# Kernel optimization log

Hardware: AMD Instinct MI355X
Metric: run time of the kernel (lower is better)

The kernel has to match this reference:

```python
import jax, jax.numpy as jnp
import numpy as np
from jax import lax

N_EXPERTS = 16
TOP_K = 2
D_MODEL = 512
D_FF = 2048


def setup_inputs() -> dict:
    key = jax.random.key(0)
    ks = jax.random.split(key, 7)
    s_in = 1.0 / np.sqrt(D_MODEL)
    s_ff = 1.0 / np.sqrt(D_FF)
    x = jax.random.normal(ks[0], (2, 2048, D_MODEL), dtype=jnp.float32)
    router_w = jax.random.uniform(ks[1], (N_EXPERTS, D_MODEL), jnp.float32, -s_in, s_in)
    router_b = jax.random.uniform(ks[2], (N_EXPERTS,), jnp.float32, -s_in, s_in)
    w1 = jax.random.uniform(ks[3], (N_EXPERTS, D_FF, D_MODEL), jnp.float32, -s_in, s_in)
    b1 = jax.random.uniform(ks[4], (N_EXPERTS, D_FF), jnp.float32, -s_in, s_in)
    w2 = jax.random.uniform(ks[5], (N_EXPERTS, D_MODEL, D_FF), jnp.float32, -s_ff, s_ff)
    b2 = jax.random.uniform(ks[6], (N_EXPERTS, D_MODEL), jnp.float32, -s_ff, s_ff)
    return {"x": x, "router_w": router_w, "router_b": router_b,
            "w1": w1, "b1": b1, "w2": w2, "b2": b2}


def reference(x, router_w, router_b, w1, b1, w2, b2):
    B, S, D = x.shape
    xt = x.reshape(-1, D)                                   # [T, D]
    logits = xt @ router_w.T + router_b                     # [T, E]
    probs = jax.nn.softmax(logits, axis=-1)
    topk_p, topk_i = lax.top_k(probs, TOP_K)                # [T, K]
    # Dense gate matrix: gate[t, e] = topk prob if expert e selected else 0.
    # Weighting by gate reproduces the masked gather/scatter-add exactly.
    onehot = jax.nn.one_hot(topk_i, N_EXPERTS, dtype=probs.dtype)  # [T, K, E]
    gates = jnp.sum(onehot * topk_p[..., None], axis=1)     # [T, E]

    def expert_step(acc, packed):
        w1e, b1e, w2e, b2e, ge = packed                     # per-expert params + gate col [T]
        h = jax.nn.gelu(xt @ w1e.T + b1e, approximate=False)  # [T, D_FF]
        y = h @ w2e.T + b2e                                 # [T, D]
        return acc + y * ge[:, None], None

    out, _ = lax.scan(expert_step, jnp.zeros_like(xt),
                      (w1, b1, w2, b2, gates.T))
    return out.reshape(B, S, D)
```

## Files before the change

kernel.cpp:

```cpp
#include <hip/hip_runtime.h>
#include <stdint.h>

#define T_TOK 4096
#define DM    512
#define DFF   2048
#define NE    16
#define NSLOT (T_TOK * 2)
#define NW    (NE * DFF * DM)
#define MAXTILE 80

typedef __attribute__((ext_vector_type(8))) short  bf16x8;
typedef __attribute__((ext_vector_type(4))) float  f32x4;
typedef __attribute__((ext_vector_type(8))) unsigned short us8;

static __device__ __forceinline__ unsigned short f2bf(float f) {
    unsigned int u = __float_as_uint(f);
    u += 0x7FFFu + ((u >> 16) & 1u);
    return (unsigned short)(u >> 16);
}

static __device__ __forceinline__ void gload_lds16(const void* g, void* l) {
    __builtin_amdgcn_global_load_lds(
        (const __attribute__((address_space(1))) void*)g,
        (__attribute__((address_space(3))) void*)l, 16, 0, 0);
}

__global__ __launch_bounds__(256) void convert_kernel(
    const float* __restrict__ w1, const float* __restrict__ w2,
    unsigned short* __restrict__ w1b, unsigned short* __restrict__ w2b)
{
    size_t i = ((size_t)blockIdx.x * 256 + threadIdx.x) * 8;
    const float* src; unsigned short* dst;
    if (i < (size_t)NW) { src = w1 + i;        dst = w1b + i; }
    else                { src = w2 + (i - NW); dst = w2b + (i - NW); }
    f32x4 a = *(const f32x4*)src;
    f32x4 b = *(const f32x4*)(src + 4);
    us8 v;
    v[0] = f2bf(a.x); v[1] = f2bf(a.y); v[2] = f2bf(a.z); v[3] = f2bf(a.w);
    v[4] = f2bf(b.x); v[5] = f2bf(b.y); v[6] = f2bf(b.z); v[7] = f2bf(b.w);
    *(us8*)dst = v;
}

__global__ __launch_bounds__(256) void router_kernel(
    const float* __restrict__ x, const float* __restrict__ rw,
    const float* __restrict__ rb, int* __restrict__ tok_e,
    float* __restrict__ tok_g, unsigned short* __restrict__ xb)
{
    __shared__ float rws[NE * DM];
    int tid = threadIdx.x;
    for (int i = 0; i < 8; ++i) {
        int idx = (tid + i * 256) * 4;
        *(f32x4*)&rws[idx] = *(const f32x4*)&rw[idx];
    }
    __syncthreads();

    int wid = tid >> 6, lane = tid & 63;
    int t = blockIdx.x * 4 + wid;

    float xv[8];
    const float* xp = x + (size_t)t * DM + lane * 8;
    *(f32x4*)&xv[0] = *(const f32x4*)xp;
    *(f32x4*)&xv[4] = *(const f32x4*)(xp + 4);

    us8 v;
    for (int i = 0; i < 8; ++i) v[i] = f2bf(xv[i]);
    *(us8*)&xb[(size_t)t * DM + lane * 8] = v;

    float acc[NE];
    for (int e = 0; e < NE; ++e) {
        const float* wp = &rws[e * DM + lane * 8];
        float a = 0.f;
        for (int i = 0; i < 8; ++i) a += xv[i] * wp[i];
        acc[e] = a;
    }
    for (int e = 0; e < NE; ++e) {
        float v2 = acc[e];
        for (int off = 32; off > 0; off >>= 1) v2 += __shfl_xor(v2, off);
        acc[e] = v2 + rb[e];
    }
    float m = acc[0];
    for (int e = 1; e < NE; ++e) m = fmaxf(m, acc[e]);
    float p[NE]; float s = 0.f;
    for (int e = 0; e < NE; ++e) { p[e] = expf(acc[e] - m); s += p[e]; }
    float inv = 1.f / s;
    int i0 = 0; float p0 = p[0];
    for (int e = 1; e < NE; ++e) if (p[e] > p0) { p0 = p[e]; i0 = e; }
    int i1 = (i0 == 0) ? 1 : 0; float p1 = p[i1];
    for (int e = 0; e < NE; ++e)
        if (e != i0 && p[e] > p1) { p1 = p[e]; i1 = e; }
    if (lane == 0) {
        tok_e[t * 2]     = i0;  tok_e[t * 2 + 1] = i1;
        tok_g[t * 2]     = p0 * inv;
        tok_g[t * 2 + 1] = p1 * inv;
    }
}

__global__ __launch_bounds__(256) void compact_kernel(
    const int* __restrict__ tok_e, int* __restrict__ slot_token,
    int* __restrict__ tok_slot, int* __restrict__ eoff)
{
    __shared__ int cnt[NE], cur[NE];
    int tid = threadIdx.x;
    if (tid < NE) cnt[tid] = 0;
    __syncthreads();
    for (int t = tid; t < T_TOK; t += 256) {
        atomicAdd(&cnt[tok_e[t * 2]], 1);
        atomicAdd(&cnt[tok_e[t * 2 + 1]], 1);
    }
    __syncthreads();
    if (tid == 0) {
        int r = 0, tb = 0;
        for (int e = 0; e < NE; ++e) {
            eoff[e] = r; cur[e] = r; r += cnt[e];
            eoff[16 + e] = cnt[e];
            eoff[32 + e] = tb; tb += (cnt[e] + 127) >> 7;
        }
        eoff[48] = tb;
    }
    __syncthreads();
    for (int t = tid; t < T_TOK; t += 256) {
        for (int k = 0; k < 2; ++k) {
            int e = tok_e[t * 2 + k];
            int s = atomicAdd(&cur[e], 1);
            slot_token[s]     = t;
            tok_slot[t * 2 + k] = s;
        }
    }
}

__global__ __launch_bounds__(256) void gemm1_kernel(
    const unsigned short* __restrict__ xb, const unsigned short* __restrict__ w1b,
    const float* __restrict__ b1, const int* __restrict__ slot_token,
    const int* __restrict__ eoff, unsigned short* __restrict__ h)
{
    __shared__ unsigned short smem[16384];
    __shared__ int tokrow[128];
    __shared__ int meta[49];
    unsigned short* As = smem;
    unsigned short* Bs = smem + 8192;

    int tid = threadIdx.x;
    if (tid < 49) meta[tid] = eoff[tid];
    __syncthreads();

    int slot_idx = blockIdx.y;
    if (slot_idx >= meta[48]) return;
    int e = 0;
    while (e < NE - 1 && meta[32 + e + 1] <= slot_idx) ++e;
    int mt  = slot_idx - meta[32 + e];
    int off = meta[e], cnt = meta[16 + e];
    int nB    = blockIdx.x * 128;
    int slot0 = off + mt * 128;
    int valid = cnt - mt * 128; if (valid > 128) valid = 128;

    if (tid < 128) {
        int s = slot0 + tid; if (s > NSLOT - 1) s = NSLOT - 1;
        tokrow[tid] = slot_token[s];
    }
    __syncthreads();

    f32x4 acc[16];
    for (int i = 0; i < 16; ++i) acc[i] = (f32x4){0.f, 0.f, 0.f, 0.f};

    const unsigned short* wb = w1b + ((size_t)e * DFF + nB) * DM;
    int wid = tid >> 6, l = tid & 63;
    int wm = (wid & 1) * 64, wn = (wid >> 1) * 64;
    int q = l >> 4, c = l & 15;

    for (int kt = 0; kt < DM / 64; ++kt) {
        for (int j = 0; j < 4; ++j) {
            int u = (wid * 4 + j) * 64 + l;
            int row = u >> 3, sc = (u & 7) ^ (row & 7);
            gload_lds16(xb + (size_t)tokrow[row] * DM + kt * 64 + sc * 8, &As[u * 8]);
        }
        for (int j = 0; j < 4; ++j) {
            int u = (wid * 4 + j) * 64 + l;
            int row = u >> 3, sc = (u & 7) ^ (row & 7);
            gload_lds16(wb + (size_t)row * DM + kt * 64 + sc * 8, &Bs[u * 8]);
        }
        __syncthreads();
        for (int ks = 0; ks < 2; ++ks) {
            int sw = ((ks * 4 + q) ^ (c & 7)) * 8;
            bf16x8 af[4], bv[4];
            for (int i = 0; i < 4; ++i) af[i] = *(bf16x8*)&As[(wm + i * 16 + c) * 64 + sw];
            for (int j = 0; j < 4; ++j) bv[j] = *(bf16x8*)&Bs[(wn + j * 16 + c) * 64 + sw];
            for (int i = 0; i < 4; ++i)
                for (int j = 0; j < 4; ++j)
                    acc[i * 4 + j] = __builtin_amdgcn_mfma_f32_16x16x32_bf16(
                        af[i], bv[j], acc[i * 4 + j], 0, 0, 0);
        }
        __syncthreads();
    }

    float bias[4];
    for (int j = 0; j < 4; ++j) bias[j] = b1[e * DFF + nB + wn + j * 16 + c];
    unsigned short* bounce = smem;
    for (int ph = 0; ph < 2; ++ph) {
        __syncthreads();
        if ((wid & 1) == ph) {
            for (int i = 0; i < 4; ++i)
                for (int j = 0; j < 4; ++j) {
                    f32x4 a = acc[i * 4 + j];
                    for (int r = 0; r < 4; ++r) {
                        int rl = i * 16 + q * 4 + r;
                        float z = a[r] + bias[j];
                        float g = 0.5f * z * (1.f + erff(z * 0.70710678118654752f));
                        bounce[rl * 136 + wn + j * 16 + c] = f2bf(g);
                    }
                }
        }
        __syncthreads();
        for (int it = 0; it < 4; ++it) {
            int u2 = it * 256 + tid;
            int row = u2 >> 4, ch = u2 & 15;
            int gr = ph * 64 + row;
            if (gr < valid)
                *(us8*)&h[(size_t)(slot0 + gr) * DFF + nB + ch * 8] =
                    *(us8*)&bounce[row * 136 + ch * 8];
        }
    }
}

__global__ __launch_bounds__(256) void gemm2_kernel(
    const unsigned short* __restrict__ h, const unsigned short* __restrict__ w2b,
    const int* __restrict__ eoff, float* __restrict__ y)
{
    __shared__ unsigned short smem[16384];
    __shared__ int meta[49];
    unsigned short* As = smem;
    unsigned short* Bs = smem + 8192;

    int tid = threadIdx.x;
    if (tid < 49) meta[tid] = eoff[tid];
    __syncthreads();

    int slot_idx = blockIdx.y;
    if (slot_idx >= meta[48]) return;
    int e = 0;
    while (e < NE - 1 && meta[32 + e + 1] <= slot_idx) ++e;
    int mt  = slot_idx - meta[32 + e];
    int off = meta[e], cnt = meta[16 + e];
    int nB    = blockIdx.x * 128;
    int slot0 = off + mt * 128;
    int valid = cnt - mt * 128; if (valid > 128) valid = 128;

    f32x4 acc[16];
    for (int i = 0; i < 16; ++i) acc[i] = (f32x4){0.f, 0.f, 0.f, 0.f};

    const unsigned short* wb = w2b + ((size_t)e * DM + nB) * DFF;
    int wid = tid >> 6, l = tid & 63;
    int wm = (wid & 1) * 64, wn = (wid >> 1) * 64;
    int q = l >> 4, c = l & 15;

    for (int kt = 0; kt < DFF / 64; ++kt) {
        for (int j = 0; j < 4; ++j) {
            int u = (wid * 4 + j) * 64 + l;
            int row = u >> 3, sc = (u & 7) ^ (row & 7);
            size_t s = slot0 + row; if (s > NSLOT - 1) s = NSLOT - 1;
            gload_lds16(h + s * DFF + kt * 64 + sc * 8, &As[u * 8]);
        }
        for (int j = 0; j < 4; ++j) {
            int u = (wid * 4 + j) * 64 + l;
            int row = u >> 3, sc = (u & 7) ^ (row & 7);
            gload_lds16(wb + (size_t)row * DFF + kt * 64 + sc * 8, &Bs[u * 8]);
        }
        __syncthreads();
        for (int ks = 0; ks < 2; ++ks) {
            int sw = ((ks * 4 + q) ^ (c & 7)) * 8;
            bf16x8 af[4], bv[4];
            for (int i = 0; i < 4; ++i) af[i] = *(bf16x8*)&As[(wm + i * 16 + c) * 64 + sw];
            for (int j = 0; j < 4; ++j) bv[j] = *(bf16x8*)&Bs[(wn + j * 16 + c) * 64 + sw];
            for (int i = 0; i < 4; ++i)
                for (int j = 0; j < 4; ++j)
                    acc[i * 4 + j] = __builtin_amdgcn_mfma_f32_16x16x32_bf16(
                        af[i], bv[j], acc[i * 4 + j], 0, 0, 0);
        }
        __syncthreads();
    }

    for (int i = 0; i < 4; ++i)
        for (int j = 0; j < 4; ++j) {
            int n = nB + wn + j * 16 + c;
            for (int r = 0; r < 4; ++r) {
                int rl = wm + i * 16 + q * 4 + r;
                if (rl < valid)
                    y[(size_t)(slot0 + rl) * DM + n] = acc[i * 4 + j][r];
            }
        }
}

__global__ __launch_bounds__(256) void combine_kernel(
    const float* __restrict__ y, const float* __restrict__ b2,
    const int* __restrict__ tok_slot, const float* __restrict__ tok_g,
    const int* __restrict__ tok_e, float* __restrict__ out)
{
    int tid = threadIdx.x;
    int t = blockIdx.x * 2 + (tid >> 7);
    int d = (tid & 127) * 4;
    int s0 = tok_slot[t * 2], s1 = tok_slot[t * 2 + 1];
    float g0 = tok_g[t * 2], g1 = tok_g[t * 2 + 1];
    int e0 = tok_e[t * 2], e1 = tok_e[t * 2 + 1];
    f32x4 y0 = *(const f32x4*)&y[(size_t)s0 * DM + d];
    f32x4 y1 = *(const f32x4*)&y[(size_t)s1 * DM + d];
    f32x4 c0 = *(const f32x4*)&b2[e0 * DM + d];
    f32x4 c1 = *(const f32x4*)&b2[e1 * DM + d];
    f32x4 o;
    for (int i = 0; i < 4; ++i) o[i] = g0 * (y0[i] + c0[i]) + g1 * (y1[i] + c1[i]);
    *(f32x4*)&out[(size_t)t * DM + d] = o;
}

extern "C" void kernel_launch(void* const* d_in, const int* in_sizes, int n_in,
                              void* d_out, int out_size, void* d_ws, size_t ws_size,
                              hipStream_t stream) {
    const float* x  = (const float*)d_in[0];
    const float* rw = (const float*)d_in[1];
    const float* rb = (const float*)d_in[2];
    const float* w1 = (const float*)d_in[3];
    const float* b1 = (const float*)d_in[4];
    const float* w2 = (const float*)d_in[5];
    const float* b2 = (const float*)d_in[6];
    float* out = (float*)d_out;

    char* ws = (char*)d_ws;
    size_t o = 0;
    unsigned short* h   = (unsigned short*)(ws + o); o += (size_t)NSLOT * DFF * 2;
    unsigned short* w1b = (unsigned short*)(ws + o); o += (size_t)NW * 2;
    unsigned short* w2b = (unsigned short*)(ws + o); o += (size_t)NW * 2;
    unsigned short* xb  = (unsigned short*)(ws + o); o += (size_t)T_TOK * DM * 2;
    int*   tok_e      = (int*)(ws + o);   o += (size_t)NSLOT * 4;
    float* tok_g      = (float*)(ws + o); o += (size_t)NSLOT * 4;
    int*   tok_slot   = (int*)(ws + o);   o += (size_t)NSLOT * 4;
    int*   slot_token = (int*)(ws + o);   o += (size_t)NSLOT * 4;
    int*   eoff       = (int*)(ws + o);
    float* y = (float*)w1b;

    convert_kernel<<<2 * NW / 8 / 256, 256, 0, stream>>>(w1, w2, w1b, w2b);
    router_kernel<<<T_TOK / 4, 256, 0, stream>>>(x, rw, rb, tok_e, tok_g, xb);
    compact_kernel<<<1, 256, 0, stream>>>(tok_e, slot_token, tok_slot, eoff);
    gemm1_kernel<<<dim3(DFF / 128, MAXTILE), 256, 0, stream>>>(
        xb, w1b, b1, slot_token, eoff, h);
    gemm2_kernel<<<dim3(DM / 128, MAXTILE), 256, 0, stream>>>(
        h, w2b, eoff, y);
    combine_kernel<<<T_TOK / 2, 256, 0, stream>>>(
        y, b2, tok_slot, tok_g, tok_e, out);
}
```

Measured before the change: 315.8 us.

## Replace LDS-staged expert GEMMs with direct-register 64-row tiles and split-K GEMM2

Both expert GEMMs drop LDS staging and barriers; each wave loads its A and B fragments straight from global memory into registers. Row tiles shrink from 128 to 64 slots, so the last tile of each expert wastes fewer rows. GEMM1 gives each wave its own 64x64 output and a private LDS bounce buffer for the GELU epilogue. GEMM2 splits K into two halves that write separate partial buffers, which the combine kernel adds together. This removes barrier stalls and raises block count, at the cost of losing A-tile sharing across waves, doing more redundant global and cache traffic, and writing an extra partial y buffer.

```diff
diff --git a/kernel.cpp b/kernel.cpp
--- a/kernel.cpp
+++ b/kernel.cpp
@@ -7,7 +7,7 @@
 #define NE    16
 #define NSLOT (T_TOK * 2)
 #define NW    (NE * DFF * DM)
-#define MAXTILE 80
+#define MAXT64 144
 
 typedef __attribute__((ext_vector_type(8))) short  bf16x8;
 typedef __attribute__((ext_vector_type(4))) float  f32x4;
@@ -17,12 +17,6 @@
     unsigned int u = __float_as_uint(f);
     u += 0x7FFFu + ((u >> 16) & 1u);
     return (unsigned short)(u >> 16);
-}
-
-static __device__ __forceinline__ void gload_lds16(const void* g, void* l) {
-    __builtin_amdgcn_global_load_lds(
-        (const __attribute__((address_space(1))) void*)g,
-        (__attribute__((address_space(3))) void*)l, 16, 0, 0);
 }
 
 __global__ __launch_bounds__(256) void convert_kernel(
@@ -113,7 +107,7 @@
         for (int e = 0; e < NE; ++e) {
             eoff[e] = r; cur[e] = r; r += cnt[e];
             eoff[16 + e] = cnt[e];
-            eoff[32 + e] = tb; tb += (cnt[e] + 127) >> 7;
+            eoff[32 + e] = tb; tb += (cnt[e] + 63) >> 6;
         }
         eoff[48] = tb;
     }
@@ -122,7 +116,7 @@
         for (int k = 0; k < 2; ++k) {
             int e = tok_e[t * 2 + k];
             int s = atomicAdd(&cur[e], 1);
-            slot_token[s]     = t;
+            slot_token[s]       = t;
             tok_slot[t * 2 + k] = s;
         }
     }
@@ -133,91 +127,87 @@
     const float* __restrict__ b1, const int* __restrict__ slot_token,
     const int* __restrict__ eoff, unsigned short* __restrict__ h)
 {
-    __shared__ unsigned short smem[16384];
-    __shared__ int tokrow[128];
-    __shared__ int meta[49];
-    unsigned short* As = smem;
-    unsigned short* Bs = smem + 8192;
-
-    int tid = threadIdx.x;
-    if (tid < 49) meta[tid] = eoff[tid];
-    __syncthreads();
-
-    int slot_idx = blockIdx.y;
-    if (slot_idx >= meta[48]) return;
+    __shared__ unsigned short bounce[4][64 * 68];
+    int tid = threadIdx.x, wave = tid >> 6, l = tid & 63;
+    int c = l & 15, q = l >> 4;
+
+    int ty = blockIdx.y;
     int e = 0;
-    while (e < NE - 1 && meta[32 + e + 1] <= slot_idx) ++e;
-    int mt  = slot_idx - meta[32 + e];
-    int off = meta[e], cnt = meta[16 + e];
-    int nB    = blockIdx.x * 128;
-    int slot0 = off + mt * 128;
-    int valid = cnt - mt * 128; if (valid > 128) valid = 128;
-
-    if (tid < 128) {
-        int s = slot0 + tid; if (s > NSLOT - 1) s = NSLOT - 1;
-        tokrow[tid] = slot_token[s];
-    }
-    __syncthreads();
+    #pragma unroll
+    for (int k = 1; k < NE; ++k) e += (eoff[32 + k] <= ty) ? 1 : 0;
+    if (ty >= eoff[48]) return;
+    int off = eoff[e], cnt = eoff[16 + e];
+    int mt  = ty - eoff[32 + e];
+    int row0  = off + mt * 64;
+    int valid = cnt - mt * 64; if (valid > 64) valid = 64;
+    int nW = blockIdx.x * 256 + wave * 64;
+
+    const unsigned short* pA[4];
+    const unsigned short* pB[4];
+    int smax = off + cnt - 1;
+    #pragma unroll
+    for (int i = 0; i < 4; ++i) {
+        int s = row0 + i * 16 + c; if (s > smax) s = smax;
+        pA[i] = xb + (size_t)slot_token[s] * DM + q * 8;
+    }
+    #pragma unroll
+    for (int j = 0; j < 4; ++j)
+        pB[j] = w1b + ((size_t)e * DFF + nW + j * 16 + c) * DM + q * 8;
 
     f32x4 acc[16];
+    #pragma unroll
     for (int i = 0; i < 16; ++i) acc[i] = (f32x4){0.f, 0.f, 0.f, 0.f};
 
-    const unsigned short* wb = w1b + ((size_t)e * DFF + nB) * DM;
-    int wid = tid >> 6, l = tid & 63;
-    int wm = (wid & 1) * 64, wn = (wid >> 1) * 64;
-    int q = l >> 4, c = l & 15;
-
+    #pragma unroll 2
     for (int kt = 0; kt < DM / 64; ++kt) {
+        bf16x8 a0[4], a1[4], b0[4], b1v[4];
+        #pragma unroll
+        for (int i = 0; i < 4; ++i) {
+            a0[i] = *(const bf16x8*)(pA[i] + kt * 64);
+            a1[i] = *(const bf16x8*)(pA[i] + kt * 64 + 32);
+        }
+        #pragma unroll
         for (int j = 0; j < 4; ++j) {
-            int u = (wid * 4 + j) * 64 + l;
-            int row = u >> 3, sc = (u & 7) ^ (row & 7);
-            gload_lds16(xb + (size_t)tokrow[row] * DM + kt * 64 + sc * 8, &As[u * 8]);
-        }
+            b0[j]  = *(const bf16x8*)(pB[j] + kt * 64);
+            b1v[j] = *(const bf16x8*)(pB[j] + kt * 64 + 32);
+        }
+        #pragma unroll
+        for (int i = 0; i < 4; ++i)
+            #pragma unroll
+            for (int j = 0; j < 4; ++j)
+                acc[i * 4 + j] = __builtin_amdgcn_mfma_f32_16x16x32_bf16(
+                    a0[i], b0[j], acc[i * 4 + j], 0, 0, 0);
+        #pragma unroll
+        for (int i = 0; i < 4; ++i)
+            #pragma unroll
+            for (int j = 0; j < 4; ++j)
+                acc[i * 4 + j] = __builtin_amdgcn_mfma_f32_16x16x32_bf16(
+                    a1[i], b1v[j], acc[i * 4 + j], 0, 0, 0);
+    }
+
+    float bias[4];
+    #pragma unroll
+    for (int j = 0; j < 4; ++j) bias[j] = b1[e * DFF + nW + j * 16 + c];
+    unsigned short* bw = bounce[wave];
+    #pragma unroll
+    for (int i = 0; i < 4; ++i)
+        #pragma unroll
         for (int j = 0; j < 4; ++j) {
-            int u = (wid * 4 + j) * 64 + l;
-            int row = u >> 3, sc = (u & 7) ^ (row & 7);
-            gload_lds16(wb + (size_t)row * DM + kt * 64 + sc * 8, &Bs[u * 8]);
-        }
-        __syncthreads();
-        for (int ks = 0; ks < 2; ++ks) {
-            int sw = ((ks * 4 + q) ^ (c & 7)) * 8;
-            bf16x8 af[4], bv[4];
-            for (int i = 0; i < 4; ++i) af[i] = *(bf16x8*)&As[(wm + i * 16 + c) * 64 + sw];
-            for (int j = 0; j < 4; ++j) bv[j] = *(bf16x8*)&Bs[(wn + j * 16 + c) * 64 + sw];
-            for (int i = 0; i < 4; ++i)
-                for (int j = 0; j < 4; ++j)
-                    acc[i * 4 + j] = __builtin_amdgcn_mfma_f32_16x16x32_bf16(
-                        af[i], bv[j], acc[i * 4 + j], 0, 0, 0);
-        }
-        __syncthreads();
-    }
-
-    float bias[4];
-    for (int j = 0; j < 4; ++j) bias[j] = b1[e * DFF + nB + wn + j * 16 + c];
-    unsigned short* bounce = smem;
-    for (int ph = 0; ph < 2; ++ph) {
-        __syncthreads();
-        if ((wid & 1) == ph) {
-            for (int i = 0; i < 4; ++i)
-                for (int j = 0; j < 4; ++j) {
-                    f32x4 a = acc[i * 4 + j];
-                    for (int r = 0; r < 4; ++r) {
-                        int rl = i * 16 + q * 4 + r;
-                        float z = a[r] + bias[j];
-                        float g = 0.5f * z * (1.f + erff(z * 0.70710678118654752f));
-                        bounce[rl * 136 + wn + j * 16 + c] = f2bf(g);
-                    }
-                }
-        }
-        __syncthreads();
-        for (int it = 0; it < 4; ++it) {
-            int u2 = it * 256 + tid;
-            int row = u2 >> 4, ch = u2 & 15;
-            int gr = ph * 64 + row;
-            if (gr < valid)
-                *(us8*)&h[(size_t)(slot0 + gr) * DFF + nB + ch * 8] =
-                    *(us8*)&bounce[row * 136 + ch * 8];
-        }
+            f32x4 a = acc[i * 4 + j];
+            #pragma unroll
+            for (int r = 0; r < 4; ++r) {
+                float z = a[r] + bias[j];
+                float g = 0.5f * z * (1.f + erff(z * 0.70710678118654752f));
+                bw[(i * 16 + q * 4 + r) * 68 + j * 16 + c] = f2bf(g);
+            }
+        }
+    __asm__ volatile("s_waitcnt lgkmcnt(0)" ::: "memory");
+    #pragma unroll
+    for (int it = 0; it < 8; ++it) {
+        int row = it * 8 + (l >> 3);
+        if (row < valid)
+            *(us8*)&h[(size_t)(row0 + row) * DFF + nW + (l & 7) * 8] =
+                *(us8*)&bw[row * 68 + (l & 7) * 8];
     }
 }
 
@@ -225,68 +215,76 @@
     const unsigned short* __restrict__ h, const unsigned short* __restrict__ w2b,
     const int* __restrict__ eoff, float* __restrict__ y)
 {
-    __shared__ unsigned short smem[16384];
-    __shared__ int meta[49];
-    unsigned short* As = smem;
-    unsigned short* Bs = smem + 8192;
-
-    int tid = threadIdx.x;
-    if (tid < 49) meta[tid] = eoff[tid];
-    __syncthreads();
-
-    int slot_idx = blockIdx.y;
-    if (slot_idx >= meta[48]) return;
+    int tid = threadIdx.x, wave = tid >> 6, l = tid & 63;
+    int c = l & 15, q = l >> 4;
+
+    int ty = blockIdx.y;
     int e = 0;
-    while (e < NE - 1 && meta[32 + e + 1] <= slot_idx) ++e;
-    int mt  = slot_idx - meta[32 + e];
-    int off = meta[e], cnt = meta[16 + e];
-    int nB    = blockIdx.x * 128;
-    int slot0 = off + mt * 128;
-    int valid = cnt - mt * 128; if (valid > 128) valid = 128;
+    #pragma unroll
+    for (int k = 1; k < NE; ++k) e += (eoff[32 + k] <= ty) ? 1 : 0;
+    if (ty >= eoff[48]) return;
+    int off = eoff[e], cnt = eoff[16 + e];
+    int mt  = ty - eoff[32 + e];
+    int row0  = off + mt * 64;
+    int valid = cnt - mt * 64; if (valid > 64) valid = 64;
+    int half = blockIdx.x >> 1;
+    int nW   = (blockIdx.x & 1) * 256 + wave * 64;
+    int k0   = half * (DFF / 2);
+
+    const unsigned short* pA[4];
+    const unsigned short* pB[4];
+    int smax = off + cnt - 1;
+    #pragma unroll
+    for (int i = 0; i < 4; ++i) {
+        int s = row0 + i * 16 + c; if (s > smax) s = smax;
+        pA[i] = h + (size_t)s * DFF + k0 + q * 8;
+    }
+    #pragma unroll
+    for (int j = 0; j < 4; ++j)
+        pB[j] = w2b + ((size_t)e * DM + nW + j * 16 + c) * DFF + k0 + q * 8;
 
     f32x4 acc[16];
+    #pragma unroll
     for (int i = 0; i < 16; ++i) acc[i] = (f32x4){0.f, 0.f, 0.f, 0.f};
 
-    const unsigned short* wb = w2b + ((size_t)e * DM + nB) * DFF;
-    int wid = tid >> 6, l = tid & 63;
-    int wm = (wid & 1) * 64, wn = (wid >> 1) * 64;
-    int q = l >> 4, c = l & 15;
-
-    for (int kt = 0; kt < DFF / 64; ++kt) {
+    #pragma unroll 2
+    for (int kt = 0; kt < (DFF / 2) / 64; ++kt) {
+        bf16x8 a0[4], a1[4], b0[4], b1v[4];
+        #pragma unroll
+        for (int i = 0; i < 4; ++i) {
+            a0[i] = *(const bf16x8*)(pA[i] + kt * 64);
+            a1[i] = *(const bf16x8*)(pA[i] + kt * 64 + 32);
+        }
+        #pragma unroll
         for (int j = 0; j < 4; ++j) {
-            int u = (wid * 4 + j) * 64 + l;
-            int row = u >> 3, sc = (u & 7) ^ (row & 7);
-            size_t s = slot0 + row; if (s > NSLOT - 1) s = NSLOT - 1;
-            gload_lds16(h + s * DFF + kt * 64 + sc * 8, &As[u * 8]);
-        }
-        for (int j = 0; j < 4; ++j) {
-            int u = (wid * 4 + j) * 64 + l;
-            int row = u >> 3, sc = (u & 7) ^ (row & 7);
-            gload_lds16(wb + (size_t)row * DFF + kt * 64 + sc * 8, &Bs[u * 8]);
-        }
-        __syncthreads();
-        for (int ks = 0; ks < 2; ++ks) {
-            int sw = ((ks * 4 + q) ^ (c & 7)) * 8;
-            bf16x8 af[4], bv[4];
-            for (int i = 0; i < 4; ++i) af[i] = *(bf16x8*)&As[(wm + i * 16 + c) * 64 + sw];
-            for (int j = 0; j < 4; ++j) bv[j] = *(bf16x8*)&Bs[(wn + j * 16 + c) * 64 + sw];
-            for (int i = 0; i < 4; ++i)
-                for (int j = 0; j < 4; ++j)
-                    acc[i * 4 + j] = __builtin_amdgcn_mfma_f32_16x16x32_bf16(
-                        af[i], bv[j], acc[i * 4 + j], 0, 0, 0);
-        }
-        __syncthreads();
-    }
-
+            b0[j]  = *(const bf16x8*)(pB[j] + kt * 64);
+            b1v[j] = *(const bf16x8*)(pB[j] + kt * 64 + 32);
+        }
+        #pragma unroll
+        for (int i = 0; i < 4; ++i)
+            #pragma unroll
+            for (int j = 0; j < 4; ++j)
+                acc[i * 4 + j] = __builtin_amdgcn_mfma_f32_16x16x32_bf16(
+                    a0[i], b0[j], acc[i * 4 + j], 0, 0, 0);
+        #pragma unroll
+        for (int i = 0; i < 4; ++i)
+            #pragma unroll
+            for (int j = 0; j < 4; ++j)
+                acc[i * 4 + j] = __builtin_amdgcn_mfma_f32_16x16x32_bf16(
+                    a1[i], b1v[j], acc[i * 4 + j], 0, 0, 0);
+    }
+
+    float* yb = y + (size_t)half * NSLOT * DM;
+    #pragma unroll
     for (int i = 0; i < 4; ++i)
-        for (int j = 0; j < 4; ++j) {
-            int n = nB + wn + j * 16 + c;
+        #pragma unroll
+        for (int j = 0; j < 4; ++j)
+            #pragma unroll
             for (int r = 0; r < 4; ++r) {
-                int rl = wm + i * 16 + q * 4 + r;
-                if (rl < valid)
-                    y[(size_t)(slot0 + rl) * DM + n] = acc[i * 4 + j][r];
+                int row = i * 16 + q * 4 + r;
+                if (row < valid)
+                    yb[(size_t)(row0 + row) * DM + nW + j * 16 + c] = acc[i * 4 + j][r];
             }
-        }
 }
 
 __global__ __launch_bounds__(256) void combine_kernel(
@@ -300,12 +298,16 @@
     int s0 = tok_slot[t * 2], s1 = tok_slot[t * 2 + 1];
     float g0 = tok_g[t * 2], g1 = tok_g[t * 2 + 1];
     int e0 = tok_e[t * 2], e1 = tok_e[t * 2 + 1];
-    f32x4 y0 = *(const f32x4*)&y[(size_t)s0 * DM + d];
-    f32x4 y1 = *(const f32x4*)&y[(size_t)s1 * DM + d];
+    const float* y1 = y + (size_t)NSLOT * DM;
+    f32x4 a0 = *(const f32x4*)&y[(size_t)s0 * DM + d];
+    f32x4 a1 = *(const f32x4*)&y1[(size_t)s0 * DM + d];
+    f32x4 b0 = *(const f32x4*)&y[(size_t)s1 * DM + d];
+    f32x4 b1v = *(const f32x4*)&y1[(size_t)s1 * DM + d];
     f32x4 c0 = *(const f32x4*)&b2[e0 * DM + d];
     f32x4 c1 = *(const f32x4*)&b2[e1 * DM + d];
     f32x4 o;
-    for (int i = 0; i < 4; ++i) o[i] = g0 * (y0[i] + c0[i]) + g1 * (y1[i] + c1[i]);
+    for (int i = 0; i < 4; ++i)
+        o[i] = g0 * (a0[i] + a1[i] + c0[i]) + g1 * (b0[i] + b1v[i] + c1[i]);
     *(f32x4*)&out[(size_t)t * DM + d] = o;
 }
 
@@ -337,9 +339,9 @@
     convert_kernel<<<2 * NW / 8 / 256, 256, 0, stream>>>(w1, w2, w1b, w2b);
     router_kernel<<<T_TOK / 4, 256, 0, stream>>>(x, rw, rb, tok_e, tok_g, xb);
     compact_kernel<<<1, 256, 0, stream>>>(tok_e, slot_token, tok_slot, eoff);
-    gemm1_kernel<<<dim3(DFF / 128, MAXTILE), 256, 0, stream>>>(
+    gemm1_kernel<<<dim3(DFF / 256, MAXT64), 256, 0, stream>>>(
         xb, w1b, b1, slot_token, eoff, h);
-    gemm2_kernel<<<dim3(DM / 128, MAXTILE), 256, 0, stream>>>(
+    gemm2_kernel<<<dim3(4, MAXT64), 256, 0, stream>>>(
         h, w2b, eoff, y);
     combine_kernel<<<T_TOK / 2, 256, 0, stream>>>(
         y, b2, tok_slot, tok_g, tok_e, out);
```

Measured after the change: 397.5 us. 25.9% more time.
